# Kernel tuning notes

Measured on AMD Instinct MI355X. Metric: run time of the kernel, lower is better.

The kernel has to match this reference:

```python
import jax, jax.numpy as jnp
import numpy as np

B, S, DIM = 1, 1024, 512
H, DH = 8, 64
CB = 32   # compress block size
SB = 32   # selection block size (== CB, so no importance remap)
NSEL, NMEM, WIN = 4, 4, 64
SCALE = DH ** -0.5
EPS = 1.1920929e-07  # torch fp32 finfo eps used by nn.RMSNorm


def _rmsnorm(x, g):
    return x * jax.lax.rsqrt(jnp.mean(x * x, -1, keepdims=True) + EPS) * g


def _rope(t):
    # lucidrains rotary: interleaved pairs, theta=10000, positions 0..n-1
    d = t.shape[-1]
    inv = 1.0 / (10000.0 ** (jnp.arange(0, d, 2, dtype=jnp.float32) / d))
    ang = jnp.arange(t.shape[-2], dtype=jnp.float32)[:, None] * inv   # [n, d/2]
    cos = jnp.repeat(jnp.cos(ang), 2, axis=-1)
    sin = jnp.repeat(jnp.sin(ang), 2, axis=-1)
    tp = t.reshape(t.shape[:-1] + (d // 2, 2))
    rot = jnp.stack((-tp[..., 1], tp[..., 0]), -1).reshape(t.shape)
    return t * cos + rot * sin


def setup_inputs():
    key = jax.random.key(0)
    ks = jax.random.split(key, 12)
    cd = CB * DH
    p = lambda k, shp: jax.random.normal(k, shp, jnp.float32) * 0.02
    return {
        'inp': jax.random.normal(ks[0], (B, S, DIM), jnp.float32),
        'norm_g': jnp.ones((DIM,), jnp.float32),
        'w_qkv': p(ks[1], (DIM, 3 * H * DH)),
        'k_pos': p(ks[2], (H, CB, DH)),
        'v_pos': p(ks[3], (H, CB, DH)),
        'kc_w1': p(ks[4], (cd, cd)), 'kc_b1': jnp.zeros((cd,), jnp.float32),
        'kc_w2': p(ks[5], (cd, DH)), 'kc_b2': jnp.zeros((DH,), jnp.float32),
        'vc_w1': p(ks[6], (cd, cd)), 'vc_b1': jnp.zeros((cd,), jnp.float32),
        'vc_w2': p(ks[7], (cd, DH)), 'vc_b2': jnp.zeros((DH,), jnp.float32),
        'mem_kv': p(ks[8], (2, H, NMEM, DH)),
        'strat_w': p(ks[9], (DIM, 3 * H)),
        'strat_b': jnp.tile(jnp.array([-2.0, -2.0, 2.0], jnp.float32), H),
        'out_w': p(ks[10], (H * DH, DIM)),
    }


def reference(inp, norm_g, w_qkv, k_pos, v_pos, kc_w1, kc_b1, kc_w2, kc_b2,
              vc_w1, vc_b1, vc_w2, vc_b2, mem_kv, strat_w, strat_b, out_w):
    NEG = -jnp.finfo(inp.dtype).max
    x = _rmsnorm(inp, norm_g)
    q, k, v = jnp.split(x @ w_qkv, 3, axis=-1)
    sh = lambda t: t.reshape(B, S, H, DH).transpose(0, 2, 1, 3)   # b h n d
    q, k, v = sh(q), sh(k), sh(v)

    # ---- compressed branch ----
    nb = S // CB
    kb = k.reshape(B, H, nb, CB, DH) + k_pos[None, :, None]
    vb = v.reshape(B, H, nb, CB, DH) + v_pos[None, :, None]
    comp = lambda t, w1, b1, w2, b2: jax.nn.relu(
        t.reshape(B, H, nb, CB * DH) @ w1 + b1) @ w2 + b2
    ck = comp(kb, kc_w1, kc_b1, kc_w2, kc_b2)                     # b h nb d
    cv = comp(vb, vc_w1, vc_b1, vc_w2, vc_b2)
    ck = jnp.concatenate([jnp.broadcast_to(mem_kv[0][None], (B, H, NMEM, DH)), ck], 2)
    cv = jnp.concatenate([jnp.broadcast_to(mem_kv[1][None], (B, H, NMEM, DH)), cv], 2)

    csim = jnp.einsum('bhid,bhjd->bhij', q, ck) * SCALE
    pos = jnp.arange(S)
    ckpos = jnp.concatenate([jnp.full((NMEM,), -1), (jnp.arange(nb) + 1) * CB - 1])
    csim = jnp.where(ckpos[None, :] < pos[:, None], csim, NEG)
    cattn = jax.nn.softmax(csim, -1)
    c_out = jnp.einsum('bhij,bhjd->bhid', cattn, cv)

    rq, rk = _rope(q), _rope(k)

    # ---- fine selected branch (CB == SB => importance maps 1:1) ----
    imp = cattn[..., NMEM:]                                       # b h i nb
    sel_vals, sel_idx = jax.lax.top_k(imp, NSEL)                  # b h i k
    own = pos // SB
    sel_idx = jnp.concatenate(
        [sel_idx, jnp.broadcast_to(own[None, None, :, None], (B, H, S, 1))], -1)
    fmask = jnp.broadcast_to((sel_vals > 1e-10)[..., None], (B, H, S, NSEL, SB))
    causal = jnp.tril(jnp.ones((SB, SB), bool))[pos % SB]         # [S, SB]
    fmask = jnp.concatenate(
        [fmask, jnp.broadcast_to(causal[None, None, :, None, :], (B, H, S, 1, SB))], 3)
    fmask = fmask.reshape(B, H, S, (NSEL + 1) * SB)

    fkb = rk.reshape(B, H, nb, SB, DH)
    fvb = v.reshape(B, H, nb, SB, DH)
    gather = jax.vmap(jax.vmap(lambda blk, idx: blk[idx]))        # per (b,h)
    fk = gather(fkb, sel_idx).reshape(B, H, S, (NSEL + 1) * SB, DH)
    fv = gather(fvb, sel_idx).reshape(B, H, S, (NSEL + 1) * SB, DH)
    fsim = jnp.einsum('bhid,bhijd->bhij', rq, fk) * SCALE
    fattn = jax.nn.softmax(jnp.where(fmask, fsim, NEG), -1)
    f_out = jnp.einsum('bhij,bhijd->bhid', fattn, fv)

    # ---- sliding window branch (LocalAttention, causal, exact window) ----
    ssim = jnp.einsum('bhid,bhjd->bhij', rq, rk) * SCALE
    smask = (pos[None, :] <= pos[:, None]) & (pos[:, None] - pos[None, :] <= WIN)
    sattn = jax.nn.softmax(jnp.where(smask, ssim, NEG), -1)
    s_out = jnp.einsum('bhij,bhjd->bhid', sattn, v)

    # ---- gated combine ----
    strat = jax.nn.sigmoid(x @ strat_w + strat_b)
    strat = strat.reshape(B, S, H, 3).transpose(0, 2, 1, 3)       # b h n s
    out = strat[..., 0:1] * c_out + strat[..., 1:2] * f_out + strat[..., 2:3] * s_out
    return out.transpose(0, 2, 1, 3).reshape(B, S, H * DH) @ out_w
```

## Files before the change

### kernel.cpp

```cpp
#include <hip/hip_runtime.h>
#include <hip/hip_bf16.h>
#include <cfloat>
#include <math.h>

#define S_LEN 1024
#define DIM 512
#define H_N 8
#define DH 64
#define CB 32
#define NB 32
#define NSEL 4
#define NMEM 4
#define WIN 64
#define SCALE 0.125f
#define EPS 1.1920929e-07f

#define OFF_X      0u
#define OFF_RKT    0u
#define OFF_QKV    524288u
#define OFF_RQ     2097152u
#define OFF_RK     2621440u
#define OFF_VBUF   3145728u
#define OFF_CKT    3670016u
#define OFF_CVC    3702784u
#define OFF_STRAT  3735552u
#define OFF_ATT    3760128u
#define OFF_HK     4284416u
#define OFF_QKVP   5332992u
#define OFF_COMPP  5332992u
#define OFF_OUTP   5332992u

__global__ void rmsnorm_strat_k(const float* __restrict__ inp, const float* __restrict__ g,
                                const float* __restrict__ sw, const float* __restrict__ sb,
                                float* __restrict__ x, float* __restrict__ strat) {
    int s = blockIdx.x;
    int t = threadIdx.x;
    __shared__ __align__(16) float xs[512];
    __shared__ float red[24][8];
    float v0 = inp[s * DIM + t];
    float v1 = inp[s * DIM + t + 256];
    float ss = v0 * v0 + v1 * v1;
    for (int o = 32; o > 0; o >>= 1) ss += __shfl_xor(ss, o);
    __shared__ float wsum[4];
    int wid = t >> 6, lane = t & 63;
    if (lane == 0) wsum[wid] = ss;
    __syncthreads();
    float tot = wsum[0] + wsum[1] + wsum[2] + wsum[3];
    float scale = 1.0f / sqrtf(tot / (float)DIM + EPS);
    float x0 = v0 * scale * g[t];
    float x1 = v1 * scale * g[t + 256];
    x[s * DIM + t]       = x0;
    x[s * DIM + t + 256] = x1;
    xs[t] = x0;
    xs[t + 256] = x1;
    __syncthreads();
    if (t < 192) {
        int o = t >> 3, p = t & 7;
        float acc = 0.0f;
        const float* xb = xs + p * 64;
        for (int k = 0; k < 64; ++k) acc += xb[k] * sw[(p * 64 + k) * 24 + o];
        red[o][p] = acc;
    }
    __syncthreads();
    if (t < 24) {
        float a = sb[t];
        for (int p = 0; p < 8; ++p) a += red[t][p];
        strat[s * 24 + t] = 1.0f / (1.0f + expf(-a));
    }
}

__device__ __forceinline__ void gemm_sk_body(const float* __restrict__ A, const float* __restrict__ B,
                                             float* __restrict__ P, int M, int N, int K,
                                             int kstart, int Ks) {
    __shared__ __align__(16) float As[2][16][68];
    __shared__ __align__(16) float Bs[2][16][64];
    const int bm = blockIdx.x * 64, bn = blockIdx.y * 64;
    const int tid = threadIdx.x;
    const int tx = tid & 15, ty = tid >> 4;
    const int ar = tid >> 2;
    const int ac = (tid & 3) * 4;
    const int br = tid >> 4;
    const int bc = (tid & 15) * 4;
    const float* Aptr = A + (size_t)(bm + ar) * K + kstart + ac;
    const float* Bptr = B + (size_t)(kstart + br) * N + bn + bc;

    float4 a4 = *(const float4*)(Aptr);
    float4 b4 = *(const float4*)(Bptr);
    float acc[4][4] = {};
    int buf = 0;
    for (int k0 = 0; k0 < Ks; k0 += 16) {
        As[buf][ac + 0][ar] = a4.x;
        As[buf][ac + 1][ar] = a4.y;
        As[buf][ac + 2][ar] = a4.z;
        As[buf][ac + 3][ar] = a4.w;
        *(float4*)&Bs[buf][br][bc] = b4;
        __syncthreads();
        if (k0 + 16 < Ks) {
            a4 = *(const float4*)(Aptr + k0 + 16);
            b4 = *(const float4*)(Bptr + (size_t)(k0 + 16) * N);
        }
#pragma unroll
        for (int kk = 0; kk < 16; ++kk) {
            const float4 af = *(const float4*)&As[buf][kk][ty * 4];
            const float4 bf = *(const float4*)&Bs[buf][kk][tx * 4];
            acc[0][0] += af.x * bf.x; acc[0][1] += af.x * bf.y; acc[0][2] += af.x * bf.z; acc[0][3] += af.x * bf.w;
            acc[1][0] += af.y * bf.x; acc[1][1] += af.y * bf.y; acc[1][2] += af.y * bf.z; acc[1][3] += af.y * bf.w;
            acc[2][0] += af.z * bf.x; acc[2][1] += af.z * bf.y; acc[2][2] += af.z * bf.z; acc[2][3] += af.z * bf.w;
            acc[3][0] += af.w * bf.x; acc[3][1] += af.w * bf.y; acc[3][2] += af.w * bf.z; acc[3][3] += af.w * bf.w;
        }
        buf ^= 1;
    }
#pragma unroll
    for (int i = 0; i < 4; ++i) {
        int m = bm + ty * 4 + i;
        float4 v;
        v.x = acc[i][0]; v.y = acc[i][1]; v.z = acc[i][2]; v.w = acc[i][3];
        *(float4*)&P[(size_t)m * N + bn + tx * 4] = v;
    }
}

__global__ void gemm_sk_k(const float* __restrict__ A, const float* __restrict__ B,
                          float* __restrict__ P, int M, int N, int K, int nsplit) {
    int kz = blockIdx.z;
    int Ks = K / nsplit;
    gemm_sk_body(A, B, P + (size_t)kz * M * N, M, N, K, kz * Ks, Ks);
}

__global__ void reduce_qkv_k(const float* __restrict__ P, float* __restrict__ qkv,
                             float* __restrict__ vbuf) {
    int idx4 = blockIdx.x * 256 + threadIdx.x;
    const int mn4 = 393216;
    float4 v = ((const float4*)P)[idx4];
    float4 w = ((const float4*)P)[idx4 + mn4];
    v.x += w.x; v.y += w.y; v.z += w.z; v.w += w.w;
    ((float4*)qkv)[idx4] = v;
    int c = (idx4 % 384) * 4;
    if (c >= 1024) {
        int s = idx4 / 384;
        int h = (c - 1024) >> 6, d = (c - 1024) & 63;
        *(float4*)(vbuf + (size_t)h * 65536 + s * 64 + d) = v;
    }
}

__global__ void rope_apply_k(const float* __restrict__ qkv,
                             float* __restrict__ rq, float* __restrict__ rk) {
    int idx = blockIdx.x * 256 + threadIdx.x;
    int s = idx >> 8;
    int rem = idx & 255;
    int h = rem >> 5, i = rem & 31;
    double inv = pow(10000.0, -(double)i / 32.0);
    double ang = (double)s * inv;
    float c = (float)cos(ang), sn = (float)sin(ang);
    int qb = s * 1536 + h * 64 + 2 * i;
    float q0 = qkv[qb], q1 = qkv[qb + 1];
    int ob = s * 512 + h * 64 + 2 * i;
    rq[ob]     = q0 * c - q1 * sn;
    rq[ob + 1] = q1 * c + q0 * sn;
    float k0 = qkv[qb + 512], k1 = qkv[qb + 513];
    rk[ob]     = k0 * c - k1 * sn;
    rk[ob + 1] = k1 * c + k0 * sn;
}

__global__ void transpose_rk_k(const float* __restrict__ rk, float* __restrict__ rkT,
                               const float* __restrict__ mem_kv, float* __restrict__ ckT) {
    int h = blockIdx.x, st = blockIdx.y, t = threadIdx.x;
    __shared__ float tile[64][65];
    int s0 = st * 64;
    int r = t >> 2, c0 = (t & 3) * 16;
    const float* src = rk + (size_t)(s0 + r) * 512 + h * 64 + c0;
#pragma unroll
    for (int q = 0; q < 4; ++q) {
        float4 v = *(const float4*)(src + q * 4);
        tile[r][c0 + q * 4 + 0] = v.x;
        tile[r][c0 + q * 4 + 1] = v.y;
        tile[r][c0 + q * 4 + 2] = v.z;
        tile[r][c0 + q * 4 + 3] = v.w;
    }
    __syncthreads();
    int wv = t >> 6, ls = t & 63;
    float* dst = rkT + (size_t)h * 65536 + s0 + ls;
#pragma unroll
    for (int p = 0; p < 16; ++p) {
        int d = p * 4 + wv;
        dst[(size_t)d * 1024] = tile[ls][d];
    }
    if (st == 0) {
        int d = t >> 2, j = t & 3;
        ckT[h * 2304 + d * 36 + j] = mem_kv[h * 256 + j * 64 + d];
    }
}

__global__ void gemm_comp_k(const float* __restrict__ qkv, const float* __restrict__ k_pos,
                            const float* __restrict__ v_pos, const float* __restrict__ kw1,
                            const float* __restrict__ vw1, float* __restrict__ P) {
    int z = blockIdx.z, g = z >> 2, kz = z & 3;
    const float* B = g ? vw1 : kw1;
    const float* pos = g ? v_pos : k_pos;
    const int qoff = g ? 1024 : 512;
    const int kstart = kz * 512;
    __shared__ __align__(16) float As[2][16][68];
    __shared__ __align__(16) float Bs[2][16][64];
    const int bm = blockIdx.x * 64, bn = blockIdx.y * 64;
    const int tid = threadIdx.x;
    const int tx = tid & 15, ty = tid >> 4;
    const int ar = tid >> 2, ac = (tid & 3) * 4;
    const int br = tid >> 4, bc = (tid & 15) * 4;
    const int m = bm + ar;
    const int hh = m >> 5, nb = m & 31;
    const float* qb = qkv + (size_t)(nb * 32) * 1536 + qoff + hh * 64;
    const float* pb = pos + hh * 2048;
    const float* Bptr = B + (size_t)(kstart + br) * 2048 + bn + bc;

    auto loadA = [&](int kk) {
        int cb = kk >> 6, d = kk & 63;
        float4 a = *(const float4*)(qb + (size_t)cb * 1536 + d);
        float4 p = *(const float4*)(pb + cb * 64 + d);
        a.x += p.x; a.y += p.y; a.z += p.z; a.w += p.w;
        return a;
    };

    float4 a4 = loadA(kstart + ac);
    float4 b4 = *(const float4*)Bptr;
    float acc[4][4] = {};
    int buf = 0;
    for (int k0 = 0; k0 < 512; k0 += 16) {
        As[buf][ac + 0][ar] = a4.x;
        As[buf][ac + 1][ar] = a4.y;
        As[buf][ac + 2][ar] = a4.z;
        As[buf][ac + 3][ar] = a4.w;
        *(float4*)&Bs[buf][br][bc] = b4;
        __syncthreads();
        if (k0 + 16 < 512) {
            a4 = loadA(kstart + ac + k0 + 16);
            b4 = *(const float4*)(Bptr + (size_t)(k0 + 16) * 2048);
        }
#pragma unroll
        for (int kk = 0; kk < 16; ++kk) {
            const float4 af = *(const float4*)&As[buf][kk][ty * 4];
            const float4 bf = *(const float4*)&Bs[buf][kk][tx * 4];
            acc[0][0] += af.x * bf.x; acc[0][1] += af.x * bf.y; acc[0][2] += af.x * bf.z; acc[0][3] += af.x * bf.w;
            acc[1][0] += af.y * bf.x; acc[1][1] += af.y * bf.y; acc[1][2] += af.y * bf.z; acc[1][3] += af.y * bf.w;
            acc[2][0] += af.z * bf.x; acc[2][1] += af.z * bf.y; acc[2][2] += af.z * bf.z; acc[2][3] += af.z * bf.w;
            acc[3][0] += af.w * bf.x; acc[3][1] += af.w * bf.y; acc[3][2] += af.w * bf.z; acc[3][3] += af.w * bf.w;
        }
        buf ^= 1;
    }
    float* Pz = P + (size_t)z * 524288;
#pragma unroll
    for (int i = 0; i < 4; ++i) {
        int mm = bm + ty * 4 + i;
        float4 v;
        v.x = acc[i][0]; v.y = acc[i][1]; v.z = acc[i][2]; v.w = acc[i][3];
        *(float4*)&Pz[(size_t)mm * 2048 + bn + tx * 4] = v;
    }
}

__global__ void reduce_comp_k(const float* __restrict__ P, const float* __restrict__ kb,
                              const float* __restrict__ vb, float* __restrict__ hkv) {
    int idx4 = blockIdx.x * 256 + threadIdx.x;
    const int half4 = 131072;
    int which = idx4 >= half4 ? 1 : 0;
    int l4 = idx4 - which * half4;
    const float4* p4 = (const float4*)P + (size_t)which * 4 * half4 + l4;
    float4 v = p4[0];
    float4 w1 = p4[half4], w2 = p4[2 * half4], w3 = p4[3 * (size_t)half4];
    v.x += w1.x + w2.x + w3.x; v.y += w1.y + w2.y + w3.y;
    v.z += w1.z + w2.z + w3.z; v.w += w1.w + w2.w + w3.w;
    int col = (l4 * 4) & 2047;
    const float* bias = (which ? vb : kb) + col;
    v.x = fmaxf(v.x + bias[0], 0.f); v.y = fmaxf(v.y + bias[1], 0.f);
    v.z = fmaxf(v.z + bias[2], 0.f); v.w = fmaxf(v.w + bias[3], 0.f);
    *(float4*)(hkv + (size_t)which * 524288 + (size_t)l4 * 4) = v;
}

template <int NS>
__global__ void reduce_k(const float* __restrict__ P, float* __restrict__ Y, int MN) {
    int idx4 = blockIdx.x * 256 + threadIdx.x;
    if (idx4 * 4 >= MN) return;
    const float4* p4 = (const float4*)P;
    int mn4 = MN >> 2;
    float4 v = p4[idx4];
#pragma unroll
    for (int j = 1; j < NS; ++j) {
        float4 w = p4[idx4 + (size_t)j * mn4];
        v.x += w.x; v.y += w.y; v.z += w.z; v.w += w.w;
    }
    ((float4*)Y)[idx4] = v;
}

__global__ void gemm_skinny_z2_k(const float* __restrict__ hkv, const float* __restrict__ kw2,
                                 const float* __restrict__ kb2, const float* __restrict__ vw2,
                                 const float* __restrict__ vb2, float* __restrict__ ckT,
                                 float* __restrict__ cvc) {
    int z = blockIdx.z;
    const float* A = hkv + (size_t)z * 524288;
    const float* B = z ? vw2 : kw2;
    const float* bias = z ? vb2 : kb2;
    int row = blockIdx.x;
    int col = threadIdx.x & 63;
    int chunk = threadIdx.x >> 6;
    const float* a = A + (size_t)row * 2048 + chunk * 512;
    const float* b = B + (size_t)chunk * 512 * 64;
    float acc = 0.0f;
    for (int k = 0; k < 512; k += 4) {
        float4 av = *(const float4*)(a + k);
        acc += av.x * b[(k + 0) * 64 + col];
        acc += av.y * b[(k + 1) * 64 + col];
        acc += av.z * b[(k + 2) * 64 + col];
        acc += av.w * b[(k + 3) * 64 + col];
    }
    __shared__ float red[4][64];
    red[chunk][col] = acc;
    __syncthreads();
    if (chunk == 0) {
        float v = red[0][col] + red[1][col] + red[2][col] + red[3][col] + bias[col];
        int hh = row >> 5, j = row & 31;
        if (z == 0) ckT[hh * 2304 + col * 36 + 4 + j] = v;
        else        cvc[(size_t)row * 64 + col] = v;
    }
}

__device__ __forceinline__ float redmax64(float v) {
    for (int o = 32; o > 0; o >>= 1) v = fmaxf(v, __shfl_xor(v, o));
    return v;
}
__device__ __forceinline__ float redsum64(float v) {
    for (int o = 32; o > 0; o >>= 1) v += __shfl_xor(v, o);
    return v;
}

__global__ __launch_bounds__(64) void attn_fused_k(
    const float* __restrict__ qkv, const float* __restrict__ rq,
    const float* __restrict__ rkT, const float* __restrict__ ckT,
    const float* __restrict__ cvc, const float* __restrict__ mem_kv,
    const float* __restrict__ vbuf, const float* __restrict__ strat,
    float* __restrict__ att) {
    int s = blockIdx.x, h = blockIdx.y, lane = threadIdx.x;
    __shared__ __align__(16) float qs[64];
    __shared__ __align__(16) float rqs[64];
    __shared__ float paw[192];
    __shared__ int rww[192];
    qs[lane]  = qkv[s * 1536 + h * 64 + lane];
    rqs[lane] = rq[s * 512 + h * 64 + lane];
    __syncthreads();

    int own = s >> 5, p = s & 31, t31 = lane & 31;
    bool hiw = lane >= 32;
    int lo = (s > WIN) ? s - WIN : 0;
    int cnt = s - lo + 1;
    bool cvalid = (lane < NMEM) || (lane < 36 && (lane - NMEM + 1) * CB - 1 < s);
    int jc = (lane < 36) ? lane : 35;
    int rowC = own * 32 + t31;
    int rowSA = lo + lane;      if (rowSA > 1023) rowSA = 1023;
    int rowSB = lo + 64 + lane; if (rowSB > 1023) rowSB = 1023;
    const float* rkTh = rkT + (size_t)h * 65536;
    const float* ckTh = ckT + h * 2304;

    float c0 = 0, c1 = 0, f0 = 0, f1 = 0, a0 = 0, a1 = 0, b0 = 0, b1 = 0;
#pragma unroll 4
    for (int d = 0; d < 64; d += 2) {
        float qd0 = qs[d], qd1 = qs[d + 1];
        float rd0 = rqs[d], rd1 = rqs[d + 1];
        const float* r0 = rkTh + (size_t)d * 1024;
        const float* r1 = r0 + 1024;
        c0 += qd0 * ckTh[d * 36 + jc];
        c1 += qd1 * ckTh[(d + 1) * 36 + jc];
        f0 += rd0 * r0[rowC];  f1 += rd1 * r1[rowC];
        a0 += rd0 * r0[rowSA]; a1 += rd1 * r1[rowSA];
        b0 += rd0 * r0[rowSB]; b1 += rd1 * r1[rowSB];
    }

    float simc = cvalid ? (c0 + c1) * SCALE : -FLT_MAX;
    float mx = redmax64(simc);
    float e = (simc == -FLT_MAX) ? 0.0f : expf(simc - mx);
    float tot = redsum64(e);
    float a = e / tot;
    paw[lane] = (lane < 36) ? a : 0.0f;
    __syncthreads();
    float cacc;
    {
        const float* mv = mem_kv + 2048 + h * 256 + lane;
        cacc = paw[0] * mv[0] + paw[1] * mv[64] + paw[2] * mv[128] + paw[3] * mv[192];
        const float* cvb = cvc + h * 2048 + lane;
        for (int j = 0; j < 32; ++j) cacc += paw[4 + j] * cvb[j * 64];
    }

    float tval = (lane >= NMEM && lane < 36) ? a : -1.0f;
    int tidx = lane - NMEM;
    int sel0, sel1, sel2, sel3, msk = 0;
#pragma unroll
    for (int t = 0; t < NSEL; ++t) {
        float bv = tval; int bi = tidx;
        for (int o = 32; o > 0; o >>= 1) {
            float ov = __shfl_xor(bv, o);
            int oi = __shfl_xor(bi, o);
            if (ov > bv || (ov == bv && oi < bi)) { bv = ov; bi = oi; }
        }
        if (t == 0) sel0 = bi; else if (t == 1) sel1 = bi;
        else if (t == 2) sel2 = bi; else sel3 = bi;
        if (bv > 1e-10f) msk |= 1 << t;
        if (tidx == bi && lane >= NMEM && lane < 36) tval = -1.0f;
    }

    int rowA = (hiw ? sel1 : sel0) * 32 + t31;
    int rowB = (hiw ? sel3 : sel2) * 32 + t31;
    float A0 = 0, A1 = 0, B0 = 0, B1 = 0;
#pragma unroll 4
    for (int d = 0; d < 64; d += 2) {
        float rd0 = rqs[d], rd1 = rqs[d + 1];
        const float* r0 = rkTh + (size_t)d * 1024;
        const float* r1 = r0 + 1024;
        A0 += rd0 * r0[rowA]; A1 += rd1 * r1[rowA];
        B0 += rd0 * r0[rowB]; B1 += rd1 * r1[rowB];
    }
    bool valA = hiw ? ((msk >> 1) & 1) : (msk & 1);
    bool valB = hiw ? ((msk >> 3) & 1) : ((msk >> 2) & 1);
    bool valC = (!hiw) && (t31 <= p);
    float simA = valA ? (A0 + A1) * SCALE : -FLT_MAX;
    float simB = valB ? (B0 + B1) * SCALE : -FLT_MAX;
    float simC = valC ? (f0 + f1) * SCALE : -FLT_MAX;

    float fmx = redmax64(fmaxf(fmaxf(simA, simB), simC));
    float eA = (simA == -FLT_MAX) ? 0.0f : expf(simA - fmx);
    float eB = (simB == -FLT_MAX) ? 0.0f : expf(simB - fmx);
    float eC = (simC == -FLT_MAX) ? 0.0f : expf(simC - fmx);
    float fsum = redsum64(eA + eB + eC);
    float finv = 1.0f / fsum;
    __syncthreads();
    paw[lane] = eA * finv;        rww[lane] = rowA;
    paw[64 + lane] = eB * finv;   rww[64 + lane] = rowB;
    paw[128 + lane] = eC * finv;  rww[128 + lane] = rowC;
    __syncthreads();
    const float* vh = vbuf + (size_t)h * 65536 + lane;
    float facc = 0.0f;
    for (int kk = 0; kk < 160; ++kk) {
        float w = paw[kk];
        if (w != 0.0f) facc += w * vh[(size_t)rww[kk] * 64];
    }
    __syncthreads();

    float sA = (lane < cnt) ? (a0 + a1) * SCALE : -FLT_MAX;
    float sB = (64 + lane < cnt) ? (b0 + b1) * SCALE : -FLT_MAX;
    float smx = redmax64(fmaxf(sA, sB));
    float esA = (sA == -FLT_MAX) ? 0.0f : expf(sA - smx);
    float esB = (sB == -FLT_MAX) ? 0.0f : expf(sB - smx);
    float ssum = redsum64(esA + esB);
    float sinv = 1.0f / ssum;
    paw[lane] = esA * sinv;
    if (64 + lane < cnt) paw[64 + lane] = esB * sinv;
    __syncthreads();
    float sacc = 0.0f;
    const float* vlo = vh + (size_t)lo * 64;
    for (int kk = 0; kk < cnt; ++kk)
        sacc += paw[kk] * vlo[(size_t)kk * 64];

    const float* st = strat + s * 24 + h * 3;
    att[s * 512 + h * 64 + lane] = st[0] * cacc + st[1] * facc + st[2] * sacc;
}

extern "C" void kernel_launch(void* const* d_in, const int* in_sizes, int n_in,
                              void* d_out, int out_size, void* d_ws, size_t ws_size,
                              hipStream_t stream) {
    const float* inp     = (const float*)d_in[0];
    const float* norm_g  = (const float*)d_in[1];
    const float* w_qkv   = (const float*)d_in[2];
    const float* k_pos   = (const float*)d_in[3];
    const float* v_pos   = (const float*)d_in[4];
    const float* kc_w1   = (const float*)d_in[5];
    const float* kc_b1   = (const float*)d_in[6];
    const float* kc_w2   = (const float*)d_in[7];
    const float* kc_b2   = (const float*)d_in[8];
    const float* vc_w1   = (const float*)d_in[9];
    const float* vc_b1   = (const float*)d_in[10];
    const float* vc_w2   = (const float*)d_in[11];
    const float* vc_b2   = (const float*)d_in[12];
    const float* mem_kv  = (const float*)d_in[13];
    const float* strat_w = (const float*)d_in[14];
    const float* strat_b = (const float*)d_in[15];
    const float* out_w   = (const float*)d_in[16];
    float* out = (float*)d_out;

    float* ws = (float*)d_ws;
    float* x     = ws + OFF_X;
    float* rkT   = ws + OFF_RKT;
    float* qkv   = ws + OFF_QKV;
    float* rq    = ws + OFF_RQ;
    float* rk    = ws + OFF_RK;
    float* vbuf  = ws + OFF_VBUF;
    float* ckT   = ws + OFF_CKT;
    float* cvc   = ws + OFF_CVC;
    float* strat = ws + OFF_STRAT;
    float* att   = ws + OFF_ATT;
    float* hkv   = ws + OFF_HK;
    float* qkvp  = ws + OFF_QKVP;
    float* compp = ws + OFF_COMPP;
    float* outp  = ws + OFF_OUTP;

    rmsnorm_strat_k<<<1024, 256, 0, stream>>>(inp, norm_g, strat_w, strat_b, x, strat);
    gemm_sk_k<<<dim3(16, 24, 2), 256, 0, stream>>>(x, w_qkv, qkvp, 1024, 1536, 512, 2);
    reduce_qkv_k<<<1536, 256, 0, stream>>>(qkvp, qkv, vbuf);
    rope_apply_k<<<1024, 256, 0, stream>>>(qkv, rq, rk);
    transpose_rk_k<<<dim3(8, 16), 256, 0, stream>>>(rk, rkT, mem_kv, ckT);
    gemm_comp_k<<<dim3(4, 32, 8), 256, 0, stream>>>(qkv, k_pos, v_pos, kc_w1, vc_w1, compp);
    reduce_comp_k<<<1024, 256, 0, stream>>>(compp, kc_b1, vc_b1, hkv);
    gemm_skinny_z2_k<<<dim3(256, 1, 2), 256, 0, stream>>>(hkv, kc_w2, kc_b2, vc_w2, vc_b2, ckT, cvc);
    attn_fused_k<<<dim3(1024, 8), 64, 0, stream>>>(qkv, rq, rkT, ckT, cvc, mem_kv, vbuf, strat, att);
    gemm_sk_k<<<dim3(16, 8, 4), 256, 0, stream>>>(att, out_w, outp, 1024, 512, 512, 4);
    reduce_k<4><<<512, 256, 0, stream>>>(outp, out, 1024 * 512);
}
```

Baseline: 386.0 us.

## Drop K transpose; compute attention dots on row-major K with wave shuffles

Removes the transpose_rk_k kernel and the transposed K/compressed-K layouts. The attention kernel now does each dot product per lane over a row-major 64-float K row using float4 loads, broadcasting q through wave shuffles. Shared-memory probability arrays and barriers are replaced by shuffles, with fixed-trip unrolled loops for the selected-block and sliding-window PV sums. Four query rows are packed per 256-thread block. Per-lane float4 row reads are strided across lanes, which may coalesce worse than the old transposed access, and there are many shuffles.

```diff
diff --git a/kernel.cpp b/kernel.cpp
--- a/kernel.cpp
+++ b/kernel.cpp
@@ -16,12 +16,11 @@
 #define EPS 1.1920929e-07f
 
 #define OFF_X      0u
-#define OFF_RKT    0u
 #define OFF_QKV    524288u
 #define OFF_RQ     2097152u
 #define OFF_RK     2621440u
 #define OFF_VBUF   3145728u
-#define OFF_CKT    3670016u
+#define OFF_CKC    3670016u
 #define OFF_CVC    3702784u
 #define OFF_STRAT  3735552u
 #define OFF_ATT    3760128u
@@ -161,35 +160,6 @@
     rk[ob + 1] = k1 * c + k0 * sn;
 }
 
-__global__ void transpose_rk_k(const float* __restrict__ rk, float* __restrict__ rkT,
-                               const float* __restrict__ mem_kv, float* __restrict__ ckT) {
-    int h = blockIdx.x, st = blockIdx.y, t = threadIdx.x;
-    __shared__ float tile[64][65];
-    int s0 = st * 64;
-    int r = t >> 2, c0 = (t & 3) * 16;
-    const float* src = rk + (size_t)(s0 + r) * 512 + h * 64 + c0;
-#pragma unroll
-    for (int q = 0; q < 4; ++q) {
-        float4 v = *(const float4*)(src + q * 4);
-        tile[r][c0 + q * 4 + 0] = v.x;
-        tile[r][c0 + q * 4 + 1] = v.y;
-        tile[r][c0 + q * 4 + 2] = v.z;
-        tile[r][c0 + q * 4 + 3] = v.w;
-    }
-    __syncthreads();
-    int wv = t >> 6, ls = t & 63;
-    float* dst = rkT + (size_t)h * 65536 + s0 + ls;
-#pragma unroll
-    for (int p = 0; p < 16; ++p) {
-        int d = p * 4 + wv;
-        dst[(size_t)d * 1024] = tile[ls][d];
-    }
-    if (st == 0) {
-        int d = t >> 2, j = t & 3;
-        ckT[h * 2304 + d * 36 + j] = mem_kv[h * 256 + j * 64 + d];
-    }
-}
-
 __global__ void gemm_comp_k(const float* __restrict__ qkv, const float* __restrict__ k_pos,
                             const float* __restrict__ v_pos, const float* __restrict__ kw1,
                             const float* __restrict__ vw1, float* __restrict__ P) {
@@ -290,7 +260,7 @@
 
 __global__ void gemm_skinny_z2_k(const float* __restrict__ hkv, const float* __restrict__ kw2,
                                  const float* __restrict__ kb2, const float* __restrict__ vw2,
-                                 const float* __restrict__ vb2, float* __restrict__ ckT,
+                                 const float* __restrict__ vb2, float* __restrict__ ckc,
                                  float* __restrict__ cvc) {
     int z = blockIdx.z;
     const float* A = hkv + (size_t)z * 524288;
@@ -314,8 +284,7 @@
     __syncthreads();
     if (chunk == 0) {
         float v = red[0][col] + red[1][col] + red[2][col] + red[3][col] + bias[col];
-        int hh = row >> 5, j = row & 31;
-        if (z == 0) ckT[hh * 2304 + col * 36 + 4 + j] = v;
+        if (z == 0) ckc[(size_t)row * 64 + col] = v;
         else        cvc[(size_t)row * 64 + col] = v;
     }
 }
@@ -328,64 +297,64 @@
     for (int o = 32; o > 0; o >>= 1) v += __shfl_xor(v, o);
     return v;
 }
-
-__global__ __launch_bounds__(64) void attn_fused_k(
+__device__ __forceinline__ float bdot(float qv, const float* __restrict__ krow) {
+    const float4* k4 = (const float4*)krow;
+    float a0 = 0, a1 = 0, a2 = 0, a3 = 0;
+#pragma unroll
+    for (int i = 0; i < 4; ++i) {
+        float4 ka = k4[4 * i], kb = k4[4 * i + 1], kc = k4[4 * i + 2], kd = k4[4 * i + 3];
+        int b = 16 * i;
+        a0 += __shfl(qv, b + 0) * ka.x + __shfl(qv, b + 1) * ka.y + __shfl(qv, b + 2) * ka.z + __shfl(qv, b + 3) * ka.w;
+        a1 += __shfl(qv, b + 4) * kb.x + __shfl(qv, b + 5) * kb.y + __shfl(qv, b + 6) * kb.z + __shfl(qv, b + 7) * kb.w;
+        a2 += __shfl(qv, b + 8) * kc.x + __shfl(qv, b + 9) * kc.y + __shfl(qv, b + 10) * kc.z + __shfl(qv, b + 11) * kc.w;
+        a3 += __shfl(qv, b + 12) * kd.x + __shfl(qv, b + 13) * kd.y + __shfl(qv, b + 14) * kd.z + __shfl(qv, b + 15) * kd.w;
+    }
+    return (a0 + a1) + (a2 + a3);
+}
+
+__global__ __launch_bounds__(256) void attn_fused_k(
     const float* __restrict__ qkv, const float* __restrict__ rq,
-    const float* __restrict__ rkT, const float* __restrict__ ckT,
+    const float* __restrict__ rk, const float* __restrict__ ckc,
     const float* __restrict__ cvc, const float* __restrict__ mem_kv,
     const float* __restrict__ vbuf, const float* __restrict__ strat,
     float* __restrict__ att) {
-    int s = blockIdx.x, h = blockIdx.y, lane = threadIdx.x;
-    __shared__ __align__(16) float qs[64];
-    __shared__ __align__(16) float rqs[64];
-    __shared__ float paw[192];
-    __shared__ int rww[192];
-    qs[lane]  = qkv[s * 1536 + h * 64 + lane];
-    rqs[lane] = rq[s * 512 + h * 64 + lane];
-    __syncthreads();
-
-    int own = s >> 5, p = s & 31, t31 = lane & 31;
-    bool hiw = lane >= 32;
-    int lo = (s > WIN) ? s - WIN : 0;
-    int cnt = s - lo + 1;
+    const int lane = threadIdx.x & 63;
+    const int s = blockIdx.x * 4 + (threadIdx.x >> 6);
+    const int h = blockIdx.y;
+
+    const float qv  = qkv[s * 1536 + h * 64 + lane];
+    const float rqv = rq[s * 512 + h * 64 + lane];
+
     bool cvalid = (lane < NMEM) || (lane < 36 && (lane - NMEM + 1) * CB - 1 < s);
-    int jc = (lane < 36) ? lane : 35;
-    int rowC = own * 32 + t31;
-    int rowSA = lo + lane;      if (rowSA > 1023) rowSA = 1023;
-    int rowSB = lo + 64 + lane; if (rowSB > 1023) rowSB = 1023;
-    const float* rkTh = rkT + (size_t)h * 65536;
-    const float* ckTh = ckT + h * 2304;
-
-    float c0 = 0, c1 = 0, f0 = 0, f1 = 0, a0 = 0, a1 = 0, b0 = 0, b1 = 0;
-#pragma unroll 4
-    for (int d = 0; d < 64; d += 2) {
-        float qd0 = qs[d], qd1 = qs[d + 1];
-        float rd0 = rqs[d], rd1 = rqs[d + 1];
-        const float* r0 = rkTh + (size_t)d * 1024;
-        const float* r1 = r0 + 1024;
-        c0 += qd0 * ckTh[d * 36 + jc];
-        c1 += qd1 * ckTh[(d + 1) * 36 + jc];
-        f0 += rd0 * r0[rowC];  f1 += rd1 * r1[rowC];
-        a0 += rd0 * r0[rowSA]; a1 += rd1 * r1[rowSA];
-        b0 += rd0 * r0[rowSB]; b1 += rd1 * r1[rowSB];
-    }
-
-    float simc = cvalid ? (c0 + c1) * SCALE : -FLT_MAX;
+    int jcl = (lane < 36 && lane >= NMEM) ? lane - NMEM : 0;
+    const float* ckrow = (lane < NMEM) ? (mem_kv + (h * 4 + lane) * 64)
+                                       : (ckc + (size_t)(h * 32 + jcl) * 64);
+    float simc = bdot(qv, ckrow) * SCALE;
+    simc = cvalid ? simc : -FLT_MAX;
     float mx = redmax64(simc);
     float e = (simc == -FLT_MAX) ? 0.0f : expf(simc - mx);
     float tot = redsum64(e);
-    float a = e / tot;
-    paw[lane] = (lane < 36) ? a : 0.0f;
-    __syncthreads();
+    float ca = e / tot;
+
     float cacc;
     {
         const float* mv = mem_kv + 2048 + h * 256 + lane;
-        cacc = paw[0] * mv[0] + paw[1] * mv[64] + paw[2] * mv[128] + paw[3] * mv[192];
+        float c0 = __shfl(ca, 0) * mv[0];
+        float c1 = __shfl(ca, 1) * mv[64];
+        float c2 = __shfl(ca, 2) * mv[128];
+        float c3 = __shfl(ca, 3) * mv[192];
         const float* cvb = cvc + h * 2048 + lane;
-        for (int j = 0; j < 32; ++j) cacc += paw[4 + j] * cvb[j * 64];
-    }
-
-    float tval = (lane >= NMEM && lane < 36) ? a : -1.0f;
+#pragma unroll
+        for (int j = 0; j < 32; j += 4) {
+            c0 += __shfl(ca, 4 + j) * cvb[(j + 0) * 64];
+            c1 += __shfl(ca, 5 + j) * cvb[(j + 1) * 64];
+            c2 += __shfl(ca, 6 + j) * cvb[(j + 2) * 64];
+            c3 += __shfl(ca, 7 + j) * cvb[(j + 3) * 64];
+        }
+        cacc = (c0 + c1) + (c2 + c3);
+    }
+
+    float tval = (lane >= NMEM && lane < 36) ? ca : -1.0f;
     int tidx = lane - NMEM;
     int sel0, sel1, sel2, sel3, msk = 0;
 #pragma unroll
@@ -402,57 +371,70 @@
         if (tidx == bi && lane >= NMEM && lane < 36) tval = -1.0f;
     }
 
+    const int t31 = lane & 31;
+    const bool hiw = lane >= 32;
+    const int own = s >> 5, p = s & 31;
+    const float* rkh = rk + h * 64;
     int rowA = (hiw ? sel1 : sel0) * 32 + t31;
     int rowB = (hiw ? sel3 : sel2) * 32 + t31;
-    float A0 = 0, A1 = 0, B0 = 0, B1 = 0;
-#pragma unroll 4
-    for (int d = 0; d < 64; d += 2) {
-        float rd0 = rqs[d], rd1 = rqs[d + 1];
-        const float* r0 = rkTh + (size_t)d * 1024;
-        const float* r1 = r0 + 1024;
-        A0 += rd0 * r0[rowA]; A1 += rd1 * r1[rowA];
-        B0 += rd0 * r0[rowB]; B1 += rd1 * r1[rowB];
-    }
+    int rowC = own * 32 + t31;
+    float simA = bdot(rqv, rkh + (size_t)rowA * 512) * SCALE;
+    float simB = bdot(rqv, rkh + (size_t)rowB * 512) * SCALE;
+    float simC = bdot(rqv, rkh + (size_t)rowC * 512) * SCALE;
     bool valA = hiw ? ((msk >> 1) & 1) : (msk & 1);
     bool valB = hiw ? ((msk >> 3) & 1) : ((msk >> 2) & 1);
     bool valC = (!hiw) && (t31 <= p);
-    float simA = valA ? (A0 + A1) * SCALE : -FLT_MAX;
-    float simB = valB ? (B0 + B1) * SCALE : -FLT_MAX;
-    float simC = valC ? (f0 + f1) * SCALE : -FLT_MAX;
+    simA = valA ? simA : -FLT_MAX;
+    simB = valB ? simB : -FLT_MAX;
+    simC = valC ? simC : -FLT_MAX;
 
     float fmx = redmax64(fmaxf(fmaxf(simA, simB), simC));
     float eA = (simA == -FLT_MAX) ? 0.0f : expf(simA - fmx);
     float eB = (simB == -FLT_MAX) ? 0.0f : expf(simB - fmx);
     float eC = (simC == -FLT_MAX) ? 0.0f : expf(simC - fmx);
-    float fsum = redsum64(eA + eB + eC);
-    float finv = 1.0f / fsum;
-    __syncthreads();
-    paw[lane] = eA * finv;        rww[lane] = rowA;
-    paw[64 + lane] = eB * finv;   rww[64 + lane] = rowB;
-    paw[128 + lane] = eC * finv;  rww[128 + lane] = rowC;
-    __syncthreads();
+    float finv = 1.0f / redsum64(eA + eB + eC);
+    float pA = eA * finv, pB = eB * finv, pC = eC * finv;
+
     const float* vh = vbuf + (size_t)h * 65536 + lane;
-    float facc = 0.0f;
-    for (int kk = 0; kk < 160; ++kk) {
-        float w = paw[kk];
-        if (w != 0.0f) facc += w * vh[(size_t)rww[kk] * 64];
-    }
-    __syncthreads();
-
-    float sA = (lane < cnt) ? (a0 + a1) * SCALE : -FLT_MAX;
-    float sB = (64 + lane < cnt) ? (b0 + b1) * SCALE : -FLT_MAX;
-    float smx = redmax64(fmaxf(sA, sB));
+    float facc;
+    {
+        float f0 = 0, f1 = 0, f2 = 0, f3 = 0, f4 = 0;
+#pragma unroll
+        for (int kk = 0; kk < 32; ++kk) {
+            f0 += __shfl(pA, kk)      * vh[(sel0 * 32 + kk) * 64];
+            f1 += __shfl(pA, kk + 32) * vh[(sel1 * 32 + kk) * 64];
+            f2 += __shfl(pB, kk)      * vh[(sel2 * 32 + kk) * 64];
+            f3 += __shfl(pB, kk + 32) * vh[(sel3 * 32 + kk) * 64];
+            f4 += __shfl(pC, kk)      * vh[(own * 32 + kk) * 64];
+        }
+        facc = ((f0 + f1) + (f2 + f3)) + f4;
+    }
+
+    const int lo = (s > WIN) ? s - WIN : 0;
+    const int cnt = s - lo + 1;
+    float sA = bdot(rqv, rkh + (size_t)(lo + lane) * 512) * SCALE;
+    sA = (lane < cnt) ? sA : -FLT_MAX;
+    bool v65 = (s >= 64);
+    float s65 = bdot(rqv, rkh + (size_t)(lo + 64) * 512) * SCALE;
+    float smx = redmax64(fmaxf(sA, v65 ? s65 : -FLT_MAX));
     float esA = (sA == -FLT_MAX) ? 0.0f : expf(sA - smx);
-    float esB = (sB == -FLT_MAX) ? 0.0f : expf(sB - smx);
-    float ssum = redsum64(esA + esB);
+    float es65 = v65 ? expf(s65 - smx) : 0.0f;
+    float ssum = redsum64(esA) + es65;
     float sinv = 1.0f / ssum;
-    paw[lane] = esA * sinv;
-    if (64 + lane < cnt) paw[64 + lane] = esB * sinv;
-    __syncthreads();
-    float sacc = 0.0f;
-    const float* vlo = vh + (size_t)lo * 64;
-    for (int kk = 0; kk < cnt; ++kk)
-        sacc += paw[kk] * vlo[(size_t)kk * 64];
+    float psA = esA * sinv;
+    float sacc;
+    {
+        float s0 = 0, s1 = 0, s2 = 0, s3 = 0;
+        const float* vlo = vh + (size_t)lo * 64;
+#pragma unroll
+        for (int kk = 0; kk < 64; kk += 4) {
+            s0 += __shfl(psA, kk)     * vlo[(kk + 0) * 64];
+            s1 += __shfl(psA, kk + 1) * vlo[(kk + 1) * 64];
+            s2 += __shfl(psA, kk + 2) * vlo[(kk + 2) * 64];
+            s3 += __shfl(psA, kk + 3) * vlo[(kk + 3) * 64];
+        }
+        sacc = (s0 + s1) + (s2 + s3) + (es65 * sinv) * vlo[64 * 64];
+    }
 
     const float* st = strat + s * 24 + h * 3;
     att[s * 512 + h * 64 + lane] = st[0] * cacc + st[1] * facc + st[2] * sacc;
@@ -482,12 +464,11 @@
 
     float* ws = (float*)d_ws;
     float* x     = ws + OFF_X;
-    float* rkT   = ws + OFF_RKT;
     float* qkv   = ws + OFF_QKV;
     float* rq    = ws + OFF_RQ;
     float* rk    = ws + OFF_RK;
     float* vbuf  = ws + OFF_VBUF;
-    float* ckT   = ws + OFF_CKT;
+    float* ckc   = ws + OFF_CKC;
     float* cvc   = ws + OFF_CVC;
     float* strat = ws + OFF_STRAT;
     float* att   = ws + OFF_ATT;
@@ -500,11 +481,10 @@
     gemm_sk_k<<<dim3(16, 24, 2), 256, 0, stream>>>(x, w_qkv, qkvp, 1024, 1536, 512, 2);
     reduce_qkv_k<<<1536, 256, 0, stream>>>(qkvp, qkv, vbuf);
     rope_apply_k<<<1024, 256, 0, stream>>>(qkv, rq, rk);
-    transpose_rk_k<<<dim3(8, 16), 256, 0, stream>>>(rk, rkT, mem_kv, ckT);
     gemm_comp_k<<<dim3(4, 32, 8), 256, 0, stream>>>(qkv, k_pos, v_pos, kc_w1, vc_w1, compp);
     reduce_comp_k<<<1024, 256, 0, stream>>>(compp, kc_b1, vc_b1, hkv);
-    gemm_skinny_z2_k<<<dim3(256, 1, 2), 256, 0, stream>>>(hkv, kc_w2, kc_b2, vc_w2, vc_b2, ckT, cvc);
-    attn_fused_k<<<dim3(1024, 8), 64, 0, stream>>>(qkv, rq, rkT, ckT, cvc, mem_kv, vbuf, strat, att);
+    gemm_skinny_z2_k<<<dim3(256, 1, 2), 256, 0, stream>>>(hkv, kc_w2, kc_b2, vc_w2, vc_b2, ckc, cvc);
+    attn_fused_k<<<dim3(256, 8), 256, 0, stream>>>(qkv, rq, rk, ckc, cvc, mem_kv, vbuf, strat, att);
     gemm_sk_k<<<dim3(16, 8, 4), 256, 0, stream>>>(att, out_w, outp, 1024, 512, 512, 4);
     reduce_k<4><<<512, 256, 0, stream>>>(outp, out, 1024 * 512);
 }
```

Measured after the change: 362.8 us. 6.0% less time.
